# Kernel optimization log

Hardware: AMD Instinct MI355X
Metric: run time of the kernel (lower is better)

Reference implementation:

```python
import jax, jax.numpy as jnp
import numpy as np

D = 768
H = 12
HD = D // H
MLP = 3072
SCALE = 1.0 / np.sqrt(HD)
EPS = 1e-6


def setup_inputs() -> dict:
    key = jax.random.key(0)
    ks = jax.random.split(key, 16)
    s = 0.02
    inp = {
        "x": jax.random.normal(ks[0], (16, 1024, D), dtype=jnp.float32),
        "wq": jax.random.normal(ks[1], (D, D), dtype=jnp.float32) * s,
        "bq": jnp.zeros((D,), jnp.float32),
        "wk": jax.random.normal(ks[2], (D, D), dtype=jnp.float32) * s,
        "bk": jnp.zeros((D,), jnp.float32),
        "wv": jax.random.normal(ks[3], (D, D), dtype=jnp.float32) * s,
        "bv": jnp.zeros((D,), jnp.float32),
        "wo": jax.random.normal(ks[4], (D, D), dtype=jnp.float32) * s,
        "bo": jnp.zeros((D,), jnp.float32),
        "w1": jax.random.normal(ks[5], (D, MLP), dtype=jnp.float32) * s,
        "b1": jax.random.normal(ks[6], (MLP,), dtype=jnp.float32) * 1e-6,
        "w2": jax.random.normal(ks[7], (MLP, D), dtype=jnp.float32) * s,
        "b2": jax.random.normal(ks[8], (D,), dtype=jnp.float32) * 1e-6,
        "ln1_g": jnp.ones((D,), jnp.float32),
        "ln1_b": jnp.zeros((D,), jnp.float32),
        "ln2_g": jnp.ones((D,), jnp.float32),
        "ln2_b": jnp.zeros((D,), jnp.float32),
    }
    return inp


def layer_norm(x, g, b):
    mu = jnp.mean(x, axis=-1, keepdims=True)
    var = jnp.mean(jnp.square(x - mu), axis=-1, keepdims=True)
    return (x - mu) * jax.lax.rsqrt(var + EPS) * g + b


def block_fwd(x, wq, bq, wk, bk, wv, bv, wo, bo, w1, b1, w2, b2,
              ln1_g, ln1_b, ln2_g, ln2_b):
    B, N, _ = x.shape
    res = x
    h = layer_norm(x, ln1_g, ln1_b)
    # QKV projections, split into heads: [B, H, N, HD]
    q = (h @ wq + bq).reshape(B, N, H, HD).transpose(0, 2, 1, 3)
    k = (h @ wk + bk).reshape(B, N, H, HD).transpose(0, 2, 1, 3)
    v = (h @ wv + bv).reshape(B, N, H, HD).transpose(0, 2, 1, 3)
    scores = jnp.einsum("bhqd,bhkd->bhqk", q, k) * SCALE
    probs = jax.nn.softmax(scores, axis=-1)
    ctx = jnp.einsum("bhqk,bhkd->bhqd", probs, v)
    ctx = ctx.transpose(0, 2, 1, 3).reshape(B, N, D)
    attn_out = ctx @ wo + bo
    x = attn_out + res
    res = x
    h = layer_norm(x, ln2_g, ln2_b)
    h = jax.nn.gelu(h @ w1 + b1, approximate=False)
    h = h @ w2 + b2
    return h + res


def reference(x, wq, bq, wk, bk, wv, bv, wo, bo, w1, b1, w2, b2,
              ln1_g, ln1_b, ln2_g, ln2_b):
    return block_fwd(x, wq, bq, wk, bk, wv, bv, wo, bo, w1, b1, w2, b2,
                     ln1_g, ln1_b, ln2_g, ln2_b)
```

## Files before the change

kernel.cpp:

```cpp
#include <hip/hip_runtime.h>
#include <hip/hip_bf16.h>
#include <math.h>


#define BS   16
#define SEQ  1024
#define DIM  768
#define NH   12
#define HDM  64
#define MLPD 3072
#define NTOK (BS * SEQ)

typedef unsigned short u16;
typedef __attribute__((ext_vector_type(8))) short bf16x8;
typedef __attribute__((ext_vector_type(4))) float f32x4;

__device__ __forceinline__ float gelu_exact(float x) {
  return 0.5f * x * (1.0f + erff(x * 0.70710678118654752440f));
}
__device__ __forceinline__ u16 f2bf(float f) {
  __hip_bfloat16 h = __float2bfloat16(f);
  u16 r;
  __builtin_memcpy(&r, &h, 2);
  return r;
}
__device__ __forceinline__ u16 f2bf_sw(float f) {
  unsigned u = __float_as_uint(f);
  return (u16)((u + 0x7fffu + ((u >> 16) & 1u)) >> 16);
}

__global__ __launch_bounds__(256) void wtrans_kernel(
    const float* __restrict__ W, u16* __restrict__ Wt, int K, int N) {
  __shared__ u16 t[64][65];
  const int k0 = blockIdx.y << 6, n0 = blockIdx.x << 6;
  const int r  = threadIdx.x >> 2;
  const int c4 = (threadIdx.x & 3) << 4;
#pragma unroll
  for (int c = 0; c < 16; c += 4) {
    const float4 v = *(const float4*)(W + (size_t)(k0 + r) * N + n0 + c4 + c);
    t[r][c4 + c + 0] = f2bf_sw(v.x);
    t[r][c4 + c + 1] = f2bf_sw(v.y);
    t[r][c4 + c + 2] = f2bf_sw(v.z);
    t[r][c4 + c + 3] = f2bf_sw(v.w);
  }
  __syncthreads();
  unsigned wbuf[8];
#pragma unroll
  for (int p = 0; p < 8; ++p)
    wbuf[p] = (unsigned)t[c4 + 2 * p][r] | ((unsigned)t[c4 + 2 * p + 1][r] << 16);
  uint4* dst = (uint4*)(Wt + (size_t)(n0 + r) * K + k0 + c4);
  dst[0] = make_uint4(wbuf[0], wbuf[1], wbuf[2], wbuf[3]);
  dst[1] = make_uint4(wbuf[4], wbuf[5], wbuf[6], wbuf[7]);
}

__global__ __launch_bounds__(256) void ln_kernel(
    const float* __restrict__ x, const float* __restrict__ g,
    const float* __restrict__ b, u16* __restrict__ out) {
  const int lane = threadIdx.x & 63;
  const int wv   = threadIdx.x >> 6;
  const int tok  = (blockIdx.x << 2) + wv;
  const float4* xr = (const float4*)(x + (size_t)tok * DIM);
  float4 a0 = xr[lane], a1 = xr[lane + 64], a2 = xr[lane + 128];
  float s  = a0.x + a0.y + a0.z + a0.w + a1.x + a1.y + a1.z + a1.w
           + a2.x + a2.y + a2.z + a2.w;
  float s2 = a0.x*a0.x + a0.y*a0.y + a0.z*a0.z + a0.w*a0.w
           + a1.x*a1.x + a1.y*a1.y + a1.z*a1.z + a1.w*a1.w
           + a2.x*a2.x + a2.y*a2.y + a2.z*a2.z + a2.w*a2.w;
#pragma unroll
  for (int o = 32; o; o >>= 1) {
    s  += __shfl_xor(s,  o, 64);
    s2 += __shfl_xor(s2, o, 64);
  }
  const float mu   = s * (1.0f / DIM);
  const float rstd = rsqrtf(s2 * (1.0f / DIM) - mu * mu + 1e-6f);
  const float4* gp = (const float4*)g;
  const float4* bp = (const float4*)b;
  ushort4* op = (ushort4*)(out + (size_t)tok * DIM);
#define LN_EMIT(av, idx)                                                       \
  {                                                                            \
    const float4 gv = gp[idx]; const float4 bv = bp[idx]; ushort4 ov;          \
    ov.x = f2bf((av.x - mu) * rstd * gv.x + bv.x);                             \
    ov.y = f2bf((av.y - mu) * rstd * gv.y + bv.y);                             \
    ov.z = f2bf((av.z - mu) * rstd * gv.z + bv.z);                             \
    ov.w = f2bf((av.w - mu) * rstd * gv.w + bv.w);                             \
    op[idx] = ov;                                                              \
  }
  LN_EMIT(a0, lane);
  LN_EMIT(a1, lane + 64);
  LN_EMIT(a2, lane + 128);
#undef LN_EMIT
}

__device__ __forceinline__ void stage128x32(const u16* gtile, int ldk,
                                            u16* lds, int tid) {
#pragma unroll
  for (int i = 0; i < 2; ++i) {
    const int b = i * 4096 + tid * 16;
    const int row = b >> 6;
    const int chunk = (b >> 4) & 3;
    const u16* src = gtile + (size_t)row * ldk + chunk * 8;
    u16* dst = lds + ((i * 4096 + (tid >> 6) * 1024) >> 1);
    __builtin_amdgcn_global_load_lds((const void*)src, (void*)dst, 16, 0, 0);
  }
}

template <int EPI>
__global__ __launch_bounds__(256) void mm_kernel(
    const u16* __restrict__ A, const u16* __restrict__ Wt,
    const float* __restrict__ bias, const float* res, void* outp,
    int M, int K, int Nc) {
  __shared__ __align__(16) u16 As[2][128 * 32];
  __shared__ __align__(16) u16 Bs[2][128 * 32];
  const int tid  = threadIdx.x;
  const int lane = tid & 63;
  const int wid  = tid >> 6;
  const int wr   = (wid >> 1) << 6;
  const int wc   = (wid & 1) << 6;
  const int row0 = blockIdx.y << 7;
  const int col0 = blockIdx.x << 7;
  const int fr   = lane & 15;
  const int kch  = lane >> 4;
  const u16* Ab = A  + (size_t)row0 * K;
  const u16* Bb = Wt + (size_t)col0 * K;
  const int nkt = K >> 5;

  f32x4 acc[4][4];
#pragma unroll
  for (int i = 0; i < 4; ++i)
#pragma unroll
    for (int j = 0; j < 4; ++j) acc[i][j] = {0.f, 0.f, 0.f, 0.f};

  stage128x32(Ab, K, As[0], tid);
  stage128x32(Bb, K, Bs[0], tid);
  __syncthreads();

  int cur = 0;
  for (int kt = 0; kt < nkt; ++kt) {
    if (kt + 1 < nkt) {
      stage128x32(Ab + (kt + 1) * 32, K, As[cur ^ 1], tid);
      stage128x32(Bb + (kt + 1) * 32, K, Bs[cur ^ 1], tid);
    }
    bf16x8 af[4], bf[4];
#pragma unroll
    for (int f = 0; f < 4; ++f) {
      af[f] = *(const bf16x8*)&As[cur][(wr + (f << 4) + fr) * 32 + (kch << 3)];
      bf[f] = *(const bf16x8*)&Bs[cur][(wc + (f << 4) + fr) * 32 + (kch << 3)];
    }
#pragma unroll
    for (int i = 0; i < 4; ++i)
#pragma unroll
      for (int j = 0; j < 4; ++j)
        acc[i][j] = __builtin_amdgcn_mfma_f32_16x16x32_bf16(af[i], bf[j],
                                                            acc[i][j], 0, 0, 0);
    __syncthreads();
    cur ^= 1;
  }

  float* outf = (float*)outp;
  u16*   outb = (u16*)outp;
#pragma unroll
  for (int jf = 0; jf < 4; ++jf) {
    const int c = col0 + wc + (jf << 4) + fr;
    const float bv = bias[c];
    if (EPI == 4) {
      const int hh = c >> 6, dd = c & 63;
#pragma unroll
      for (int i = 0; i < 4; ++i) {
        const int rbase = row0 + wr + (i << 4) + ((lane >> 4) << 2);
        const int bb = rbase >> 10, n0 = rbase & 1023;
        ushort4 o;
        o.x = f2bf(acc[i][jf][0] + bv);
        o.y = f2bf(acc[i][jf][1] + bv);
        o.z = f2bf(acc[i][jf][2] + bv);
        o.w = f2bf(acc[i][jf][3] + bv);
        *(ushort4*)(outb + ((((size_t)bb * NH + hh) * HDM + dd) << 10) + n0) = o;
      }
    } else {
#pragma unroll
      for (int i = 0; i < 4; ++i) {
#pragma unroll
        for (int j = 0; j < 4; ++j) {
          const int r = row0 + wr + (i << 4) + ((lane >> 4) << 2) + j;
          float v = acc[i][jf][j] + bv;
          if (EPI == 1) v += res[(size_t)r * Nc + c];
          if (EPI == 2) v = gelu_exact(v);
          if (EPI == 3) v *= 0.125f;
          if (EPI == 1) outf[(size_t)r * Nc + c] = v;
          else          outb[(size_t)r * Nc + c] = f2bf(v);
        }
      }
    }
  }
}

__device__ __forceinline__ int swz(int row, int chunk) {
  return row * 128 + ((chunk ^ (row & 7)) << 4);
}

__global__ __launch_bounds__(256) void attn_kernel(
    const u16* __restrict__ q, const u16* __restrict__ k,
    const u16* __restrict__ vt, u16* __restrict__ ctx) {
  __shared__ __align__(16) u16 Qs[4096];
  __shared__ __align__(16) u16 Ks[4096];
  __shared__ __align__(16) u16 Vt[4096];
  __shared__ __align__(16) u16 Ps[4096];
  const int tid  = threadIdx.x;
  const int lane = tid & 63;
  const int w    = tid >> 6;
  const int fr   = lane & 15;
  const int g    = lane >> 4;
  const int qt = blockIdx.x, h = blockIdx.y, b = blockIdx.z;
  const size_t hbase = (size_t)b * SEQ * DIM + (size_t)h * HDM;
  const u16* vhd = vt + ((size_t)(b * NH + h) * HDM) * SEQ;
  const int srow = tid >> 2;
  const int sc   = (tid & 3) << 4;
  const int sch  = sc >> 3;

  {
    const u16* qp = q + hbase + (size_t)(qt * 64 + srow) * DIM + sc;
    const uint4 q0 = *(const uint4*)qp;
    const uint4 q1 = *(const uint4*)(qp + 8);
    *(uint4*)((char*)Qs + swz(srow, sch))     = q0;
    *(uint4*)((char*)Qs + swz(srow, sch + 1)) = q1;
  }

  float m_[4] = {-INFINITY, -INFINITY, -INFINITY, -INFINITY};
  float l_[4] = {0.f, 0.f, 0.f, 0.f};
  f32x4 oacc[4];
#pragma unroll
  for (int f = 0; f < 4; ++f) oacc[f] = {0.f, 0.f, 0.f, 0.f};

  for (int kt = 0; kt < SEQ / 64; ++kt) {
    __syncthreads();
    {
      const u16* kp = k + hbase + (size_t)(kt * 64 + srow) * DIM + sc;
      const uint4 k0 = *(const uint4*)kp;
      const uint4 k1 = *(const uint4*)(kp + 8);
      *(uint4*)((char*)Ks + swz(srow, sch))     = k0;
      *(uint4*)((char*)Ks + swz(srow, sch + 1)) = k1;
      const u16* vp = vhd + (size_t)srow * SEQ + kt * 64 + sc;
      const uint4 v0 = *(const uint4*)vp;
      const uint4 v1 = *(const uint4*)(vp + 8);
      *(uint4*)((char*)Vt + swz(srow, sch))     = v0;
      *(uint4*)((char*)Vt + swz(srow, sch + 1)) = v1;
    }
    __syncthreads();

    f32x4 sacc[4];
#pragma unroll
    for (int f = 0; f < 4; ++f) sacc[f] = {0.f, 0.f, 0.f, 0.f};
    bf16x8 aq[2];
#pragma unroll
    for (int s = 0; s < 2; ++s)
      aq[s] = *(const bf16x8*)((char*)Qs + swz(w * 16 + fr, s * 4 + g));
#pragma unroll
    for (int f = 0; f < 4; ++f)
#pragma unroll
      for (int s = 0; s < 2; ++s) {
        const bf16x8 bk =
            *(const bf16x8*)((char*)Ks + swz(f * 16 + fr, s * 4 + g));
        sacc[f] = __builtin_amdgcn_mfma_f32_16x16x32_bf16(aq[s], bk, sacc[f],
                                                          0, 0, 0);
      }

    float corr[4];
#pragma unroll
    for (int r = 0; r < 4; ++r) {
      float rm = fmaxf(fmaxf(sacc[0][r], sacc[1][r]),
                       fmaxf(sacc[2][r], sacc[3][r]));
#pragma unroll
      for (int o = 8; o; o >>= 1) rm = fmaxf(rm, __shfl_xor(rm, o, 64));
      const float mnew = fmaxf(m_[r], rm);
      corr[r] = __expf(m_[r] - mnew);
      float ps = 0.f;
#pragma unroll
      for (int f = 0; f < 4; ++f) {
        const float p = __expf(sacc[f][r] - mnew);
        sacc[f][r] = p;
        ps += p;
      }
#pragma unroll
      for (int o = 8; o; o >>= 1) ps += __shfl_xor(ps, o, 64);
      l_[r] = l_[r] * corr[r] + ps;
      m_[r] = mnew;
#pragma unroll
      for (int f = 0; f < 4; ++f) oacc[f][r] *= corr[r];
    }

#pragma unroll
    for (int f = 0; f < 4; ++f)
#pragma unroll
      for (int r = 0; r < 4; ++r) {
        const int row = w * 16 + g * 4 + r;
        const int col = f * 16 + fr;
        *(u16*)((char*)Ps + ((row * 128 + col * 2) ^ ((row & 7) << 4))) =
            f2bf(sacc[f][r]);
      }

    bf16x8 ap[2];
#pragma unroll
    for (int s = 0; s < 2; ++s)
      ap[s] = *(const bf16x8*)((char*)Ps + swz(w * 16 + fr, s * 4 + g));
#pragma unroll
    for (int f = 0; f < 4; ++f)
#pragma unroll
      for (int s = 0; s < 2; ++s) {
        const bf16x8 bv =
            *(const bf16x8*)((char*)Vt + swz(f * 16 + fr, s * 4 + g));
        oacc[f] = __builtin_amdgcn_mfma_f32_16x16x32_bf16(ap[s], bv, oacc[f],
                                                          0, 0, 0);
      }
  }

  float inv[4];
#pragma unroll
  for (int r = 0; r < 4; ++r) inv[r] = 1.0f / l_[r];
#pragma unroll
  for (int f = 0; f < 4; ++f)
#pragma unroll
    for (int r = 0; r < 4; ++r) {
      const int qrow = qt * 64 + w * 16 + g * 4 + r;
      ctx[hbase + (size_t)qrow * DIM + f * 16 + fr] = f2bf(oacc[f][r] * inv[r]);
    }
}

extern "C" void kernel_launch(void* const* d_in, const int* in_sizes, int n_in,
                              void* d_out, int out_size, void* d_ws,
                              size_t ws_size, hipStream_t stream) {
  const float* x    = (const float*)d_in[0];
  const float* wq   = (const float*)d_in[1];
  const float* bq   = (const float*)d_in[2];
  const float* wk   = (const float*)d_in[3];
  const float* bk   = (const float*)d_in[4];
  const float* wv   = (const float*)d_in[5];
  const float* bv   = (const float*)d_in[6];
  const float* wo   = (const float*)d_in[7];
  const float* bo   = (const float*)d_in[8];
  const float* w1   = (const float*)d_in[9];
  const float* b1   = (const float*)d_in[10];
  const float* w2   = (const float*)d_in[11];
  const float* b2   = (const float*)d_in[12];
  const float* ln1g = (const float*)d_in[13];
  const float* ln1b = (const float*)d_in[14];
  const float* ln2g = (const float*)d_in[15];
  const float* ln2b = (const float*)d_in[16];
  float* out = (float*)d_out;

  const size_t TD = (size_t)NTOK * DIM;
  const size_t S768 = (size_t)DIM * DIM;
  const size_t SMLP = (size_t)DIM * MLPD;
  u16* wtq  = (u16*)d_ws;
  u16* wtk  = wtq + S768;
  u16* wtv  = wtk + S768;
  u16* wto  = wtv + S768;
  u16* wt1  = wto + S768;
  u16* wt2  = wt1 + SMLP;
  u16* tokb = wt2 + SMLP;
  u16* big  = tokb + TD;
  u16* qb   = big;
  u16* kb   = big + TD;
  u16* vtb  = big + 2 * TD;

  const dim3 blk(256);
  wtrans_kernel<<<dim3(DIM / 64, DIM / 64), blk, 0, stream>>>(wq, wtq, DIM, DIM);
  wtrans_kernel<<<dim3(DIM / 64, DIM / 64), blk, 0, stream>>>(wk, wtk, DIM, DIM);
  wtrans_kernel<<<dim3(DIM / 64, DIM / 64), blk, 0, stream>>>(wv, wtv, DIM, DIM);
  wtrans_kernel<<<dim3(DIM / 64, DIM / 64), blk, 0, stream>>>(wo, wto, DIM, DIM);
  wtrans_kernel<<<dim3(MLPD / 64, DIM / 64), blk, 0, stream>>>(w1, wt1, DIM, MLPD);
  wtrans_kernel<<<dim3(DIM / 64, MLPD / 64), blk, 0, stream>>>(w2, wt2, MLPD, DIM);
  ln_kernel<<<dim3(NTOK / 4), blk, 0, stream>>>(x, ln1g, ln1b, tokb);
  const dim3 g768(DIM / 128, NTOK / 128);
  mm_kernel<3><<<g768, blk, 0, stream>>>(tokb, wtq, bq, nullptr, qb, NTOK, DIM, DIM);
  mm_kernel<0><<<g768, blk, 0, stream>>>(tokb, wtk, bk, nullptr, kb, NTOK, DIM, DIM);
  mm_kernel<4><<<g768, blk, 0, stream>>>(tokb, wtv, bv, nullptr, vtb, NTOK, DIM, DIM);
  attn_kernel<<<dim3(SEQ / 64, NH, BS), blk, 0, stream>>>(qb, kb, vtb, tokb);
  mm_kernel<1><<<g768, blk, 0, stream>>>(tokb, wto, bo, x, out, NTOK, DIM, DIM);
  ln_kernel<<<dim3(NTOK / 4), blk, 0, stream>>>(out, ln2g, ln2b, tokb);
  mm_kernel<2><<<dim3(MLPD / 128, NTOK / 128), blk, 0, stream>>>(
      tokb, wt1, b1, nullptr, big, NTOK, DIM, MLPD);
  mm_kernel<1><<<g768, blk, 0, stream>>>(big, wt2, b2, out, out, NTOK, MLPD, DIM);
}
```

Measured before the change: 796.7 us.

## Fuse QKV GEMMs, add XCD block swizzle, double-buffer attention K/V tiles

Merges the three Q/K/V projection GEMMs into one launch over the concatenated transposed weights (wtq, wtk, wtv are laid out contiguously), with the epilogue picking bias, scale and output layout per column block. This cuts launch count and lets each A tile be reused across a wider output. All matmul kernels also remap block IDs so neighbouring tiles land on the same XCD for better L2 reuse. The attention kernel now prefetches the next K/V tile into registers and double-buffers LDS, so global loads overlap the MFMA work. The cost is more LDS use in attention and a dependence on the Q/K/V weight buffers staying adjacent.

```diff
diff --git a/kernel.cpp b/kernel.cpp
--- a/kernel.cpp
+++ b/kernel.cpp
@@ -104,6 +104,48 @@
   }
 }
 
+__device__ __forceinline__ void xcd_swizzle(int& bx, int& by) {
+  const int nwg  = gridDim.x * gridDim.y;
+  const int orig = blockIdx.y * gridDim.x + blockIdx.x;
+  const int q8 = nwg >> 3, r8 = nwg & 7;
+  const int xcd = orig & 7, sub = orig >> 3;
+  const int wgid = (xcd < r8 ? xcd * (q8 + 1)
+                             : r8 * (q8 + 1) + (xcd - r8) * q8) + sub;
+  bx = wgid % gridDim.x;
+  by = wgid / gridDim.x;
+}
+
+__device__ __forceinline__ void mm_core(const u16* Ab, const u16* Bb, int K,
+                                        int tid, int wr, int wc, int fr,
+                                        int kch, u16 (*As)[128 * 32],
+                                        u16 (*Bs)[128 * 32], f32x4 acc[4][4]) {
+  const int nkt = K >> 5;
+  stage128x32(Ab, K, As[0], tid);
+  stage128x32(Bb, K, Bs[0], tid);
+  __syncthreads();
+  int cur = 0;
+  for (int kt = 0; kt < nkt; ++kt) {
+    if (kt + 1 < nkt) {
+      stage128x32(Ab + (kt + 1) * 32, K, As[cur ^ 1], tid);
+      stage128x32(Bb + (kt + 1) * 32, K, Bs[cur ^ 1], tid);
+    }
+    bf16x8 af[4], bf[4];
+#pragma unroll
+    for (int f = 0; f < 4; ++f) {
+      af[f] = *(const bf16x8*)&As[cur][(wr + (f << 4) + fr) * 32 + (kch << 3)];
+      bf[f] = *(const bf16x8*)&Bs[cur][(wc + (f << 4) + fr) * 32 + (kch << 3)];
+    }
+#pragma unroll
+    for (int i = 0; i < 4; ++i)
+#pragma unroll
+      for (int j = 0; j < 4; ++j)
+        acc[i][j] = __builtin_amdgcn_mfma_f32_16x16x32_bf16(af[i], bf[j],
+                                                            acc[i][j], 0, 0, 0);
+    __syncthreads();
+    cur ^= 1;
+  }
+}
+
 template <int EPI>
 __global__ __launch_bounds__(256) void mm_kernel(
     const u16* __restrict__ A, const u16* __restrict__ Wt,
@@ -116,13 +158,12 @@
   const int wid  = tid >> 6;
   const int wr   = (wid >> 1) << 6;
   const int wc   = (wid & 1) << 6;
-  const int row0 = blockIdx.y << 7;
-  const int col0 = blockIdx.x << 7;
+  int bx, by;
+  xcd_swizzle(bx, by);
+  const int row0 = by << 7;
+  const int col0 = bx << 7;
   const int fr   = lane & 15;
   const int kch  = lane >> 4;
-  const u16* Ab = A  + (size_t)row0 * K;
-  const u16* Bb = Wt + (size_t)col0 * K;
-  const int nkt = K >> 5;
 
   f32x4 acc[4][4];
 #pragma unroll
@@ -130,31 +171,8 @@
 #pragma unroll
     for (int j = 0; j < 4; ++j) acc[i][j] = {0.f, 0.f, 0.f, 0.f};
 
-  stage128x32(Ab, K, As[0], tid);
-  stage128x32(Bb, K, Bs[0], tid);
-  __syncthreads();
-
-  int cur = 0;
-  for (int kt = 0; kt < nkt; ++kt) {
-    if (kt + 1 < nkt) {
-      stage128x32(Ab + (kt + 1) * 32, K, As[cur ^ 1], tid);
-      stage128x32(Bb + (kt + 1) * 32, K, Bs[cur ^ 1], tid);
-    }
-    bf16x8 af[4], bf[4];
-#pragma unroll
-    for (int f = 0; f < 4; ++f) {
-      af[f] = *(const bf16x8*)&As[cur][(wr + (f << 4) + fr) * 32 + (kch << 3)];
-      bf[f] = *(const bf16x8*)&Bs[cur][(wc + (f << 4) + fr) * 32 + (kch << 3)];
-    }
-#pragma unroll
-    for (int i = 0; i < 4; ++i)
-#pragma unroll
-      for (int j = 0; j < 4; ++j)
-        acc[i][j] = __builtin_amdgcn_mfma_f32_16x16x32_bf16(af[i], bf[j],
-                                                            acc[i][j], 0, 0, 0);
-    __syncthreads();
-    cur ^= 1;
-  }
+  mm_core(A + (size_t)row0 * K, Wt + (size_t)col0 * K, K, tid, wr, wc, fr,
+          kch, As, Bs, acc);
 
   float* outf = (float*)outp;
   u16*   outb = (u16*)outp;
@@ -162,33 +180,79 @@
   for (int jf = 0; jf < 4; ++jf) {
     const int c = col0 + wc + (jf << 4) + fr;
     const float bv = bias[c];
-    if (EPI == 4) {
+#pragma unroll
+    for (int i = 0; i < 4; ++i) {
+#pragma unroll
+      for (int j = 0; j < 4; ++j) {
+        const int r = row0 + wr + (i << 4) + ((lane >> 4) << 2) + j;
+        float v = acc[i][jf][j] + bv;
+        if (EPI == 1) v += res[(size_t)r * Nc + c];
+        if (EPI == 2) v = gelu_exact(v);
+        if (EPI == 1) outf[(size_t)r * Nc + c] = v;
+        else          outb[(size_t)r * Nc + c] = f2bf(v);
+      }
+    }
+  }
+}
+
+__global__ __launch_bounds__(256) void mmqkv_kernel(
+    const u16* __restrict__ A, const u16* __restrict__ Wt,
+    const float* __restrict__ bq, const float* __restrict__ bk,
+    const float* __restrict__ bv, u16* __restrict__ qb,
+    u16* __restrict__ kb, u16* __restrict__ vtb) {
+  __shared__ __align__(16) u16 As[2][128 * 32];
+  __shared__ __align__(16) u16 Bs[2][128 * 32];
+  const int tid  = threadIdx.x;
+  const int lane = tid & 63;
+  const int wid  = tid >> 6;
+  const int wr   = (wid >> 1) << 6;
+  const int wc   = (wid & 1) << 6;
+  int bx, by;
+  xcd_swizzle(bx, by);
+  const int row0 = by << 7;
+  const int col0 = bx << 7;
+  const int fr   = lane & 15;
+  const int kch  = lane >> 4;
+
+  f32x4 acc[4][4];
+#pragma unroll
+  for (int i = 0; i < 4; ++i)
+#pragma unroll
+    for (int j = 0; j < 4; ++j) acc[i][j] = {0.f, 0.f, 0.f, 0.f};
+
+  mm_core(A + (size_t)row0 * DIM, Wt + (size_t)col0 * DIM, DIM, tid, wr, wc,
+          fr, kch, As, Bs, acc);
+
+  const int sel = col0 >= 1536 ? 2 : (col0 >= 768 ? 1 : 0);
+  const float* bias = sel == 0 ? bq : (sel == 1 ? bk : bv);
+  const int cbase = col0 - sel * 768;
+#pragma unroll
+  for (int jf = 0; jf < 4; ++jf) {
+    const int c = cbase + wc + (jf << 4) + fr;
+    const float bvv = bias[c];
+    if (sel == 2) {
       const int hh = c >> 6, dd = c & 63;
 #pragma unroll
       for (int i = 0; i < 4; ++i) {
         const int rbase = row0 + wr + (i << 4) + ((lane >> 4) << 2);
         const int bb = rbase >> 10, n0 = rbase & 1023;
         ushort4 o;
-        o.x = f2bf(acc[i][jf][0] + bv);
-        o.y = f2bf(acc[i][jf][1] + bv);
-        o.z = f2bf(acc[i][jf][2] + bv);
-        o.w = f2bf(acc[i][jf][3] + bv);
-        *(ushort4*)(outb + ((((size_t)bb * NH + hh) * HDM + dd) << 10) + n0) = o;
+        o.x = f2bf(acc[i][jf][0] + bvv);
+        o.y = f2bf(acc[i][jf][1] + bvv);
+        o.z = f2bf(acc[i][jf][2] + bvv);
+        o.w = f2bf(acc[i][jf][3] + bvv);
+        *(ushort4*)(vtb + ((((size_t)bb * NH + hh) * HDM + dd) << 10) + n0) = o;
       }
     } else {
-#pragma unroll
-      for (int i = 0; i < 4; ++i) {
+      u16* dst = sel == 0 ? qb : kb;
+      const float sc = sel == 0 ? 0.125f : 1.0f;
+#pragma unroll
+      for (int i = 0; i < 4; ++i)
 #pragma unroll
         for (int j = 0; j < 4; ++j) {
           const int r = row0 + wr + (i << 4) + ((lane >> 4) << 2) + j;
-          float v = acc[i][jf][j] + bv;
-          if (EPI == 1) v += res[(size_t)r * Nc + c];
-          if (EPI == 2) v = gelu_exact(v);
-          if (EPI == 3) v *= 0.125f;
-          if (EPI == 1) outf[(size_t)r * Nc + c] = v;
-          else          outb[(size_t)r * Nc + c] = f2bf(v);
+          dst[(size_t)r * DIM + c] = f2bf((acc[i][jf][j] + bvv) * sc);
         }
-      }
     }
   }
 }
@@ -201,8 +265,8 @@
     const u16* __restrict__ q, const u16* __restrict__ k,
     const u16* __restrict__ vt, u16* __restrict__ ctx) {
   __shared__ __align__(16) u16 Qs[4096];
-  __shared__ __align__(16) u16 Ks[4096];
-  __shared__ __align__(16) u16 Vt[4096];
+  __shared__ __align__(16) u16 Ks[2][4096];
+  __shared__ __align__(16) u16 Vt[2][4096];
   __shared__ __align__(16) u16 Ps[4096];
   const int tid  = threadIdx.x;
   const int lane = tid & 63;
@@ -223,6 +287,19 @@
     *(uint4*)((char*)Qs + swz(srow, sch))     = q0;
     *(uint4*)((char*)Qs + swz(srow, sch + 1)) = q1;
   }
+  {
+    const u16* kp = k + hbase + (size_t)srow * DIM + sc;
+    const u16* vp = vhd + (size_t)srow * SEQ + sc;
+    const uint4 k0 = *(const uint4*)kp;
+    const uint4 k1 = *(const uint4*)(kp + 8);
+    const uint4 v0 = *(const uint4*)vp;
+    const uint4 v1 = *(const uint4*)(vp + 8);
+    *(uint4*)((char*)Ks[0] + swz(srow, sch))     = k0;
+    *(uint4*)((char*)Ks[0] + swz(srow, sch + 1)) = k1;
+    *(uint4*)((char*)Vt[0] + swz(srow, sch))     = v0;
+    *(uint4*)((char*)Vt[0] + swz(srow, sch + 1)) = v1;
+  }
+  __syncthreads();
 
   float m_[4] = {-INFINITY, -INFINITY, -INFINITY, -INFINITY};
   float l_[4] = {0.f, 0.f, 0.f, 0.f};
@@ -230,21 +307,20 @@
 #pragma unroll
   for (int f = 0; f < 4; ++f) oacc[f] = {0.f, 0.f, 0.f, 0.f};
 
+  int cur = 0;
   for (int kt = 0; kt < SEQ / 64; ++kt) {
-    __syncthreads();
-    {
-      const u16* kp = k + hbase + (size_t)(kt * 64 + srow) * DIM + sc;
-      const uint4 k0 = *(const uint4*)kp;
-      const uint4 k1 = *(const uint4*)(kp + 8);
-      *(uint4*)((char*)Ks + swz(srow, sch))     = k0;
-      *(uint4*)((char*)Ks + swz(srow, sch + 1)) = k1;
-      const u16* vp = vhd + (size_t)srow * SEQ + kt * 64 + sc;
-      const uint4 v0 = *(const uint4*)vp;
-      const uint4 v1 = *(const uint4*)(vp + 8);
-      *(uint4*)((char*)Vt + swz(srow, sch))     = v0;
-      *(uint4*)((char*)Vt + swz(srow, sch + 1)) = v1;
-    }
-    __syncthreads();
+    const bool pf = (kt + 1 < SEQ / 64);
+    uint4 ka, kb2, va, vb2;
+    if (pf) {
+      const u16* kp = k + hbase + (size_t)((kt + 1) * 64 + srow) * DIM + sc;
+      const u16* vp = vhd + (size_t)srow * SEQ + (kt + 1) * 64 + sc;
+      ka  = *(const uint4*)kp;
+      kb2 = *(const uint4*)(kp + 8);
+      va  = *(const uint4*)vp;
+      vb2 = *(const uint4*)(vp + 8);
+    }
+    const u16* ksc = Ks[cur];
+    const u16* vtc = Vt[cur];
 
     f32x4 sacc[4];
 #pragma unroll
@@ -258,7 +334,7 @@
 #pragma unroll
       for (int s = 0; s < 2; ++s) {
         const bf16x8 bk =
-            *(const bf16x8*)((char*)Ks + swz(f * 16 + fr, s * 4 + g));
+            *(const bf16x8*)((char*)ksc + swz(f * 16 + fr, s * 4 + g));
         sacc[f] = __builtin_amdgcn_mfma_f32_16x16x32_bf16(aq[s], bk, sacc[f],
                                                           0, 0, 0);
       }
@@ -306,10 +382,21 @@
 #pragma unroll
       for (int s = 0; s < 2; ++s) {
         const bf16x8 bv =
-            *(const bf16x8*)((char*)Vt + swz(f * 16 + fr, s * 4 + g));
+            *(const bf16x8*)((char*)vtc + swz(f * 16 + fr, s * 4 + g));
         oacc[f] = __builtin_amdgcn_mfma_f32_16x16x32_bf16(ap[s], bv, oacc[f],
                                                           0, 0, 0);
       }
+
+    if (pf) {
+      u16* ksn = Ks[cur ^ 1];
+      u16* vtn = Vt[cur ^ 1];
+      *(uint4*)((char*)ksn + swz(srow, sch))     = ka;
+      *(uint4*)((char*)ksn + swz(srow, sch + 1)) = kb2;
+      *(uint4*)((char*)vtn + swz(srow, sch))     = va;
+      *(uint4*)((char*)vtn + swz(srow, sch + 1)) = vb2;
+      __syncthreads();
+    }
+    cur ^= 1;
   }
 
   float inv[4];
@@ -369,11 +456,10 @@
   wtrans_kernel<<<dim3(MLPD / 64, DIM / 64), blk, 0, stream>>>(w1, wt1, DIM, MLPD);
   wtrans_kernel<<<dim3(DIM / 64, MLPD / 64), blk, 0, stream>>>(w2, wt2, MLPD, DIM);
   ln_kernel<<<dim3(NTOK / 4), blk, 0, stream>>>(x, ln1g, ln1b, tokb);
+  mmqkv_kernel<<<dim3(18, NTOK / 128), blk, 0, stream>>>(
+      tokb, wtq, bq, bk, bv, qb, kb, vtb);
+  attn_kernel<<<dim3(SEQ / 64, NH, BS), blk, 0, stream>>>(qb, kb, vtb, tokb);
   const dim3 g768(DIM / 128, NTOK / 128);
-  mm_kernel<3><<<g768, blk, 0, stream>>>(tokb, wtq, bq, nullptr, qb, NTOK, DIM, DIM);
-  mm_kernel<0><<<g768, blk, 0, stream>>>(tokb, wtk, bk, nullptr, kb, NTOK, DIM, DIM);
-  mm_kernel<4><<<g768, blk, 0, stream>>>(tokb, wtv, bv, nullptr, vtb, NTOK, DIM, DIM);
-  attn_kernel<<<dim3(SEQ / 64, NH, BS), blk, 0, stream>>>(qb, kb, vtb, tokb);
   mm_kernel<1><<<g768, blk, 0, stream>>>(tokb, wto, bo, x, out, NTOK, DIM, DIM);
   ln_kernel<<<dim3(NTOK / 4), blk, 0, stream>>>(out, ln2g, ln2b, tokb);
   mm_kernel<2><<<dim3(MLPD / 128, NTOK / 128), blk, 0, stream>>>(
```

Measured after the change: 772.5 us. 1.03x faster.
